# Optimization experiments

Measured on AMD Instinct MI355X. Metric: run time of the kernel, lower is better.

## Reference

```python
import jax, jax.numpy as jnp
import numpy as np

B, NU, NT = 128, 32, 64          # batch, users/sample, antennas/sample
IN_F, H, OUT_F, NL = 128, 128, 16, 2
N_U, N_A = B * NU, B * NT        # total user / antenna nodes


def setup_inputs() -> dict:
    key = jax.random.key(0)
    ks = iter(jax.random.split(key, 40))
    p = lambda shape: jax.random.normal(next(ks), shape, jnp.float32) * 0.05
    inp = {
        'user_feat': jax.random.normal(next(ks), (N_U, IN_F), jnp.float32),
        'ant_noise': jax.random.normal(next(ks), (N_A, H), jnp.float32),
    }
    # complete bipartite edges within each batch sample
    b = np.arange(B)[:, None, None]
    u = np.arange(NU)[None, :, None]
    t = np.arange(NT)[None, None, :]
    su = np.broadcast_to(b * NU + u, (B, NU, NT)).reshape(-1)  # user global ids
    dt = np.broadcast_to(b * NT + t, (B, NU, NT)).reshape(-1)  # antenna global ids
    inp['src_u2a'] = jnp.asarray(su, jnp.int32)
    inp['dst_u2a'] = jnp.asarray(dt, jnp.int32)
    inp['src_a2u'] = jnp.asarray(dt, jnp.int32)
    inp['dst_a2u'] = jnp.asarray(su, jnp.int32)
    inp['W_ue'] = p((IN_F, H)); inp['b_ue'] = p((H,))
    inp['W_t'] = p((H, H));     inp['b_t'] = p((H,))
    for name in ['ca_aggr', 'ca_self', 'ca_comb', 'cu_aggr', 'cu_self', 'cu_comb']:
        inp[name + '_W'] = p((NL, H, H))
        inp[name + '_b'] = p((NL, H))
    inp['W_norm'] = p((H, OUT_F)); inp['b_norm'] = p((OUT_F,))
    return inp


def mlp(x, W, b):
    # stack of NL Linear(H,H) + ReLU, as in MLP module
    for i in range(W.shape[0]):
        x = jax.nn.relu(x @ W[i] + b[i])
    return x


def rel_conv(src_f, dst_f, src_idx, dst_idx, n_dst, aW, ab, sW, sb, cW, cb):
    # GraphConv2: mean-aggregate mlp_aggr(src) over in-edges, combine with mlp_self(dst)
    msg = mlp(src_f, aW, ab)                                   # [n_src, H]
    summed = jax.ops.segment_sum(msg[src_idx], dst_idx, num_segments=n_dst)
    deg = jax.ops.segment_sum(jnp.ones(dst_idx.shape, jnp.float32), dst_idx,
                              num_segments=n_dst)
    mean = summed / jnp.maximum(deg, 1.0)[:, None]
    return mlp(mlp(dst_f, sW, sb) + mean, cW, cb)


def reference(user_feat, ant_noise, src_u2a, dst_u2a, src_a2u, dst_a2u,
              W_ue, b_ue, W_t, b_t,
              ca_aggr_W, ca_aggr_b, ca_self_W, ca_self_b, ca_comb_W, ca_comb_b,
              cu_aggr_W, cu_aggr_b, cu_self_W, cu_self_b, cu_comb_W, cu_comb_b,
              W_norm, b_norm):
    # InitLayer
    hu = jax.nn.relu(user_feat @ W_ue + b_ue)                  # [B*NU, H]
    ant = jax.nn.relu(hu.reshape(B, NU, H).mean(axis=1) @ W_t + b_t)  # [B, H]
    ha = jnp.repeat(ant, NT, axis=0) + ant_noise               # [B*NT, H]
    # two applications of the SAME HeteroGraphConv (shared weights)
    for _ in range(2):
        na = rel_conv(hu, ha, src_u2a, dst_u2a, N_A,
                      ca_aggr_W, ca_aggr_b, ca_self_W, ca_self_b, ca_comb_W, ca_comb_b)
        nu = rel_conv(ha, hu, src_a2u, dst_a2u, N_U,
                      cu_aggr_W, cu_aggr_b, cu_self_W, cu_self_b, cu_comb_W, cu_comb_b)
        hu, ha = nu, na
    # NormLayer: project, split real/imag, normalize to unit modulus
    y = (ha @ W_norm + b_norm).reshape(B, NT, OUT_F)
    rf = OUT_F // 2
    re, im = y[..., :rf], y[..., rf:]
    mag = jnp.sqrt(re * re + im * im)
    return jnp.concatenate([re / mag, im / mag], axis=-1)      # [B, NT, OUT_F]
```

## Files before the change

kernel.cpp:

```cpp
#include <hip/hip_runtime.h>
#include <math.h>


using frag  = __attribute__((ext_vector_type(8))) short;
using f32x4 = __attribute__((ext_vector_type(4))) float;

#define LDST 136
#define SCOPE_AGT __HIP_MEMORY_SCOPE_AGENT

__device__ __forceinline__ float  bf2f(ushort u) { return __uint_as_float(((unsigned)u) << 16); }
__device__ __forceinline__ ushort f2bf(float f) {
    unsigned u = __float_as_uint(f);
    u += 0x7fff + ((u >> 16) & 1);
    return (ushort)(u >> 16);
}
__device__ __forceinline__ unsigned cvtpk(float lo, float hi) {
    unsigned r;
    asm("v_cvt_pk_bf16_f32 %0, %1, %2" : "=v"(r) : "v"(lo), "v"(hi));
    return r;
}
__device__ __forceinline__ void gst16_sc(void* p, f32x4 v) {
    asm volatile("global_store_dwordx4 %0, %1, off sc1" :: "v"(p), "v"(v) : "memory");
}

struct GP {
    const float *uf, *noise, *b_ue, *W_t, *b_t;
    const float *bias6[6];
    const float *Wn, *bn;
    const ushort *Wp;
    float *out;
    float *pE, *pA0, *pU0, *pA1;
    unsigned *flg;
};

struct PrepP { const float* Wm[13]; ushort* Wp; unsigned* flg; };

__global__ __launch_bounds__(512) void k_prep(PrepP Q)
{
    const int tid = threadIdx.x, blk = blockIdx.x;
    if (blk < 16) Q.flg[blk * 512 + tid] = 0;
    const int e = (blk * 512 + tid) * 8;
    const int l = (e >> 3) & 63, w = (e >> 9) & 7, kc = (e >> 12) & 3, m = e >> 14;
    const float* src = Q.Wm[m] + (kc * 32 + (l >> 4) * 8) * 128 + w * 16 + (l & 15);
    ushort h[8];
#pragma unroll
    for (int j = 0; j < 8; ++j) h[j] = f2bf(src[j * 128]);
    uint4 o = { (unsigned)h[0] | ((unsigned)h[1] << 16), (unsigned)h[2] | ((unsigned)h[3] << 16),
                (unsigned)h[4] | ((unsigned)h[5] << 16), (unsigned)h[6] | ((unsigned)h[7] << 16) };
    *(uint4*)(Q.Wp + e) = o;
}

__device__ __forceinline__ void psync(unsigned* myf, unsigned* pf, unsigned s) {
    asm volatile("s_waitcnt vmcnt(0)" ::: "memory");
    __syncthreads();
    if (threadIdx.x == 0) {
        __hip_atomic_store(myf, s, __ATOMIC_RELAXED, SCOPE_AGT);
        while (__hip_atomic_load(pf, __ATOMIC_RELAXED, SCOPE_AGT) < s)
            __builtin_amdgcn_s_sleep(1);
    }
    __syncthreads();
}

struct AF { frag f[4]; };
__device__ __forceinline__ AF ldA(const ushort* __restrict__ Wp, int mat, int tid)
{
    AF a;
    const ushort* base = Wp + ((size_t)mat << 14) + (tid << 3);
#pragma unroll
    for (int kc = 0; kc < 4; ++kc)
        a.f[kc] = *(const frag*)(base + (kc << 12));
    return a;
}

template<int MT, bool MEANADD, bool CS>
__device__ __forceinline__ void mlp_stage(const AF& A, const ushort* Xl, ushort* Yl,
    const float* biasL, const float* meanL, float* csL, float* __restrict__ csG,
    int n0, int l15, int q)
{
    const float4 bv = *(const float4*)(biasL + n0 + q * 4);
    float4 mv = {0.f, 0.f, 0.f, 0.f};
    if (MEANADD) mv = *(const float4*)(meanL + n0 + q * 4);
    float cs0 = 0.f, cs1 = 0.f, cs2 = 0.f, cs3 = 0.f;
#pragma unroll
    for (int mt = 0; mt < MT; ++mt) {
        frag Bv[4];
#pragma unroll
        for (int kc = 0; kc < 4; ++kc)
            Bv[kc] = *(const frag*)(Xl + (mt * 16 + l15) * LDST + kc * 32 + q * 8);
        f32x4 acc = {0.f, 0.f, 0.f, 0.f};
#pragma unroll
        for (int kc = 0; kc < 4; ++kc)
            acc = __builtin_amdgcn_mfma_f32_16x16x32_bf16(A.f[kc], Bv[kc], acc, 0, 0, 0);
        float v0 = acc[0] + bv.x, v1 = acc[1] + bv.y, v2 = acc[2] + bv.z, v3 = acc[3] + bv.w;
        v0 = v0 > 0.f ? v0 : 0.f; v1 = v1 > 0.f ? v1 : 0.f;
        v2 = v2 > 0.f ? v2 : 0.f; v3 = v3 > 0.f ? v3 : 0.f;
        if (MEANADD) { v0 += mv.x; v1 += mv.y; v2 += mv.z; v3 += mv.w; }
        if (CS) { cs0 += v0; cs1 += v1; cs2 += v2; cs3 += v3; }
        uint2 o = { cvtpk(v0, v1), cvtpk(v2, v3) };
        *(uint2*)(Yl + (mt * 16 + l15) * LDST + n0 + q * 4) = o;
    }
    if (CS) {
#pragma unroll
        for (int m = 1; m <= 8; m <<= 1) {
            cs0 += __shfl_xor(cs0, m); cs1 += __shfl_xor(cs1, m);
            cs2 += __shfl_xor(cs2, m); cs3 += __shfl_xor(cs3, m);
        }
        if (l15 == 0) {
            f32x4 t = { cs0, cs1, cs2, cs3 };
            *(f32x4*)(csL + n0 + q * 4) = t;
            gst16_sc(csG + n0 + q * 4, t);
        }
    }
}

__global__ __launch_bounds__(512, 1) void k_gnn(GP P)
{
    __shared__ __align__(16) ushort HU[16 * LDST];
    __shared__ __align__(16) ushort HA[32 * LDST];
    __shared__ __align__(16) ushort T0[32 * LDST];
    __shared__ __align__(16) ushort T1[32 * LDST];
    __shared__ __align__(16) float  biasL[1792];
    __shared__ __align__(16) float  redL[512];
    __shared__ __align__(16) float  meanP[128], meanQ[128], antL[128];

    const int blk = blockIdx.x, tid = threadIdx.x;
    const int b = blk & 127, half = blk >> 7, prt = blk ^ 128;
    const int lane = tid & 63, wave = tid >> 6;
    const int q = lane >> 4, l15 = lane & 15;
    const int n0 = wave * 16;
    unsigned* myf = P.flg + blk * 32;
    unsigned* prf = P.flg + prt * 32;

    AF An = ldA(P.Wp, 12, tid);

    {
        const int r = tid >> 5, k4 = tid & 31;
        const float4 v = *(const float4*)(P.uf + (size_t)(b * 32 + half * 16 + r) * 128 + k4 * 4);
        uint2 o = { cvtpk(v.x, v.y), cvtpk(v.z, v.w) };
        *(uint2*)(T0 + r * LDST + k4 * 4) = o;
    }
#pragma unroll
    for (int c = tid; c < 1024; c += 512) {
        const int r = c >> 5, k4 = c & 31;
        const float4 v = *(const float4*)(P.noise + (size_t)(b * 64 + half * 32 + r) * 128 + k4 * 4);
        uint2 o = { cvtpk(v.x, v.y), cvtpk(v.z, v.w) };
        *(uint2*)(HA + r * LDST + k4 * 4) = o;
    }
    if (tid < 128) biasL[tid] = P.b_ue[tid];
    if (tid < 128) biasL[1664 + tid] = P.b_t[tid];
#pragma unroll
    for (int r = 0; r < 6; ++r)
        if (tid < 256) biasL[128 + r * 256 + tid] = P.bias6[r][tid];
    __syncthreads();

    AF A;
    A = An; An = ldA(P.Wp, 0, tid);
    mlp_stage<1, false, true>(A, T0, HU, biasL + 0, nullptr, meanP, P.pE + blk * 128, n0, l15, q);
    __syncthreads();
    A = An; An = ldA(P.Wp, 1, tid);
    mlp_stage<1, false, false>(A, HU, T0, biasL + 128, nullptr, nullptr, nullptr, n0, l15, q);
    __syncthreads();
    A = An; An = ldA(P.Wp, 6, tid);
    mlp_stage<1, false, true>(A, T0, T1, biasL + 256, nullptr, meanQ, P.pA0 + blk * 128, n0, l15, q);
    __syncthreads();
    psync(myf, prf, 1u);

    if (tid < 128) {
        meanP[tid] = (meanP[tid] + P.pE[prt * 128 + tid]) * (1.f / 32.f);
        meanQ[tid] = (meanQ[tid] + P.pA0[prt * 128 + tid]) * (1.f / 32.f);
    }
    __syncthreads();
    {
        const int g = tid >> 7, col = tid & 127;
        float s = 0.f;
#pragma unroll 4
        for (int k = g * 32; k < g * 32 + 32; ++k) s += meanP[k] * P.W_t[k * 128 + col];
        redL[g * 128 + col] = s;
    }
    __syncthreads();
    if (tid < 128) {
        float a = biasL[1664 + tid] + redL[tid] + redL[128 + tid] + redL[256 + tid] + redL[384 + tid];
        antL[tid] = a > 0.f ? a : 0.f;
    }
    __syncthreads();
#pragma unroll
    for (int c = tid; c < 1024; c += 512) {
        const int r = c >> 5, k4 = c & 31;
        ushort4 h = *(ushort4*)(HA + r * LDST + k4 * 4);
        uint2 o = { cvtpk(bf2f(h.x) + antL[k4 * 4 + 0], bf2f(h.y) + antL[k4 * 4 + 1]),
                    cvtpk(bf2f(h.z) + antL[k4 * 4 + 2], bf2f(h.w) + antL[k4 * 4 + 3]) };
        *(uint2*)(HA + r * LDST + k4 * 4) = o;
    }
    __syncthreads();

    A = An; An = ldA(P.Wp, 7, tid);
    mlp_stage<2, false, false>(A, HA, T0, biasL + 896, nullptr, nullptr, nullptr, n0, l15, q);
    __syncthreads();
    A = An; An = ldA(P.Wp, 2, tid);
    mlp_stage<2, false, true>(A, T0, T1, biasL + 1024, nullptr, meanP, P.pU0 + blk * 128, n0, l15, q);
    __syncthreads();
    A = An; An = ldA(P.Wp, 3, tid);
    mlp_stage<2, false, false>(A, HA, T0, biasL + 384, nullptr, nullptr, nullptr, n0, l15, q);
    __syncthreads();
    psync(myf, prf, 2u);
    if (tid < 128)
        meanP[tid] = (meanP[tid] + P.pU0[prt * 128 + tid]) * (1.f / 64.f);
    __syncthreads();
    A = An; An = ldA(P.Wp, 4, tid);
    mlp_stage<2, true , false>(A, T0, T1, biasL + 512, meanQ, nullptr, nullptr, n0, l15, q);
    __syncthreads();
    A = An; An = ldA(P.Wp, 5, tid);
    mlp_stage<2, false, false>(A, T1, T0, biasL + 640, nullptr, nullptr, nullptr, n0, l15, q);
    __syncthreads();
    A = An; An = ldA(P.Wp, 8, tid);
    mlp_stage<2, false, false>(A, T0, HA, biasL + 768, nullptr, nullptr, nullptr, n0, l15, q);
    __syncthreads();
    A = An; An = ldA(P.Wp, 9, tid);
    mlp_stage<1, false, false>(A, HU, T0, biasL + 1152, nullptr, nullptr, nullptr, n0, l15, q);
    __syncthreads();
    A = An; An = ldA(P.Wp, 10, tid);
    mlp_stage<1, true , false>(A, T0, T1, biasL + 1280, meanP, nullptr, nullptr, n0, l15, q);
    __syncthreads();
    A = An; An = ldA(P.Wp, 11, tid);
    mlp_stage<1, false, false>(A, T1, T0, biasL + 1408, nullptr, nullptr, nullptr, n0, l15, q);
    __syncthreads();
    A = An; An = ldA(P.Wp, 0, tid);
    mlp_stage<1, false, false>(A, T0, HU, biasL + 1536, nullptr, nullptr, nullptr, n0, l15, q);
    __syncthreads();

    A = An; An = ldA(P.Wp, 1, tid);
    mlp_stage<1, false, false>(A, HU, T0, biasL + 128, nullptr, nullptr, nullptr, n0, l15, q);
    __syncthreads();
    A = An; An = ldA(P.Wp, 2, tid);
    mlp_stage<1, false, true>(A, T0, T1, biasL + 256, nullptr, meanQ, P.pA1 + blk * 128, n0, l15, q);
    __syncthreads();
    A = An; An = ldA(P.Wp, 3, tid);
    mlp_stage<2, false, false>(A, HA, T0, biasL + 384, nullptr, nullptr, nullptr, n0, l15, q);
    __syncthreads();
    psync(myf, prf, 3u);
    if (tid < 128)
        meanQ[tid] = (meanQ[tid] + P.pA1[prt * 128 + tid]) * (1.f / 32.f);
    __syncthreads();
    A = An; An = ldA(P.Wp, 4, tid);
    mlp_stage<2, true , false>(A, T0, T1, biasL + 512, meanQ, nullptr, nullptr, n0, l15, q);
    __syncthreads();
    A = An; An = ldA(P.Wp, 5, tid);
    mlp_stage<2, false, false>(A, T1, T0, biasL + 640, nullptr, nullptr, nullptr, n0, l15, q);
    __syncthreads();
    A = An;
    mlp_stage<2, false, false>(A, T0, T1, biasL + 768, nullptr, nullptr, nullptr, n0, l15, q);
    __syncthreads();

    float* WnS = (float*)T0;
    *(float4*)(WnS + tid * 4) = *(const float4*)(P.Wn + tid * 4);
    __syncthreads();
    {
        const int row = tid >> 4, j = tid & 15;
        float acc = P.bn[j];
        const uint4* h4 = (const uint4*)(T1 + row * LDST);
#pragma unroll
        for (int kb = 0; kb < 16; ++kb) {
            const uint4 u = h4[kb];
            const float* wp = WnS + kb * 128 + j;
            acc += bf2f((ushort)u.x) * wp[0]   + bf2f((ushort)(u.x >> 16)) * wp[16]
                 + bf2f((ushort)u.y) * wp[32]  + bf2f((ushort)(u.y >> 16)) * wp[48]
                 + bf2f((ushort)u.z) * wp[64]  + bf2f((ushort)(u.z >> 16)) * wp[80]
                 + bf2f((ushort)u.w) * wp[96]  + bf2f((ushort)(u.w >> 16)) * wp[112];
        }
        const float other = __shfl_xor(acc, 8);
        const float mag = sqrtf(acc * acc + other * other);
        P.out[(size_t)(b * 64 + half * 32 + row) * 16 + j] = acc / mag;
    }
}

extern "C" void kernel_launch(void* const* d_in, const int* in_sizes, int n_in,
                              void* d_out, int out_size, void* d_ws, size_t ws_size,
                              hipStream_t stream)
{
    GP P;
    P.uf    = (const float*)d_in[0];
    P.noise = (const float*)d_in[1];
    const float* W_ue = (const float*)d_in[6];
    P.b_ue  = (const float*)d_in[7];
    P.W_t   = (const float*)d_in[8];
    P.b_t   = (const float*)d_in[9];
    const float* caW[3] = {(const float*)d_in[10], (const float*)d_in[12], (const float*)d_in[14]};
    const float* cab[3] = {(const float*)d_in[11], (const float*)d_in[13], (const float*)d_in[15]};
    const float* cuW[3] = {(const float*)d_in[16], (const float*)d_in[18], (const float*)d_in[20]};
    const float* cub[3] = {(const float*)d_in[17], (const float*)d_in[19], (const float*)d_in[21]};
    P.Wn  = (const float*)d_in[22];
    P.bn  = (const float*)d_in[23];
    P.out = (float*)d_out;

    PrepP Q;
    Q.Wm[0]  = caW[0]; Q.Wm[1]  = caW[0] + 16384;
    Q.Wm[2]  = caW[1]; Q.Wm[3]  = caW[1] + 16384;
    Q.Wm[4]  = caW[2]; Q.Wm[5]  = caW[2] + 16384;
    Q.Wm[6]  = cuW[0]; Q.Wm[7]  = cuW[0] + 16384;
    Q.Wm[8]  = cuW[1]; Q.Wm[9]  = cuW[1] + 16384;
    Q.Wm[10] = cuW[2]; Q.Wm[11] = cuW[2] + 16384;
    Q.Wm[12] = W_ue;
    P.bias6[0] = cab[0]; P.bias6[1] = cab[1]; P.bias6[2] = cab[2];
    P.bias6[3] = cub[0]; P.bias6[4] = cub[1]; P.bias6[5] = cub[2];

    char* w = (char*)d_ws;
    P.flg = (unsigned*)w;
    P.pE  = (float*)(w + 32768);
    P.pA0 = P.pE  + 256 * 128;
    P.pU0 = P.pA0 + 256 * 128;
    P.pA1 = P.pU0 + 256 * 128;
    ushort* Wp = (ushort*)(w + 32768 + 4 * 256 * 128 * 4);
    Q.Wp = Wp;
    Q.flg = P.flg;
    P.Wp = Wp;

    k_prep<<<dim3(52), dim3(512), 0, stream>>>(Q);
    k_gnn<<<dim3(256), dim3(512), 0, stream>>>(P);
}
```

Before: 120.6 us.

## Split each batch sample across four workgroups instead of two

Each sample's work is now split across four cooperating workgroups instead of two, giving 512 blocks. Each block handles 8 users and 16 antennas, and column-sum partials are exchanged through a four-way flag sync. The goal is to fill more of the GPU's compute units and shorten the serial MLP chain per block. In exchange, user-side MFMA tiles are half empty (8 valid rows out of 16), more blocks take part in each sync, and per-sample global partial traffic grows.

New measurement: 126.8 us. +5.2%, slower.

```diff
diff --git a/kernel.cpp b/kernel.cpp
--- a/kernel.cpp
+++ b/kernel.cpp
@@ -38,7 +38,7 @@
 __global__ __launch_bounds__(512) void k_prep(PrepP Q)
 {
     const int tid = threadIdx.x, blk = blockIdx.x;
-    if (blk < 16) Q.flg[blk * 512 + tid] = 0;
+    if (blk < 32) Q.flg[blk * 512 + tid] = 0;
     const int e = (blk * 512 + tid) * 8;
     const int l = (e >> 3) & 63, w = (e >> 9) & 7, kc = (e >> 12) & 3, m = e >> 14;
     const float* src = Q.Wm[m] + (kc * 32 + (l >> 4) * 8) * 128 + w * 16 + (l & 15);
@@ -50,11 +50,13 @@
     *(uint4*)(Q.Wp + e) = o;
 }
 
-__device__ __forceinline__ void psync(unsigned* myf, unsigned* pf, unsigned s) {
+__device__ __forceinline__ void psync4(unsigned* flg, int blk, unsigned s) {
     asm volatile("s_waitcnt vmcnt(0)" ::: "memory");
     __syncthreads();
-    if (threadIdx.x == 0) {
-        __hip_atomic_store(myf, s, __ATOMIC_RELAXED, SCOPE_AGT);
+    if (threadIdx.x < 3) {
+        if (threadIdx.x == 0)
+            __hip_atomic_store(flg + blk * 32, s, __ATOMIC_RELAXED, SCOPE_AGT);
+        unsigned* pf = flg + (((blk + 128 * (threadIdx.x + 1)) & 511) * 32);
         while (__hip_atomic_load(pf, __ATOMIC_RELAXED, SCOPE_AGT) < s)
             __builtin_amdgcn_s_sleep(1);
     }
@@ -72,7 +74,7 @@
     return a;
 }
 
-template<int MT, bool MEANADD, bool CS>
+template<int VALID, bool MEANADD, bool CS>
 __device__ __forceinline__ void mlp_stage(const AF& A, const ushort* Xl, ushort* Yl,
     const float* biasL, const float* meanL, float* csL, float* __restrict__ csG,
     int n0, int l15, int q)
@@ -80,26 +82,26 @@
     const float4 bv = *(const float4*)(biasL + n0 + q * 4);
     float4 mv = {0.f, 0.f, 0.f, 0.f};
     if (MEANADD) mv = *(const float4*)(meanL + n0 + q * 4);
-    float cs0 = 0.f, cs1 = 0.f, cs2 = 0.f, cs3 = 0.f;
-#pragma unroll
-    for (int mt = 0; mt < MT; ++mt) {
-        frag Bv[4];
-#pragma unroll
-        for (int kc = 0; kc < 4; ++kc)
-            Bv[kc] = *(const frag*)(Xl + (mt * 16 + l15) * LDST + kc * 32 + q * 8);
-        f32x4 acc = {0.f, 0.f, 0.f, 0.f};
-#pragma unroll
-        for (int kc = 0; kc < 4; ++kc)
-            acc = __builtin_amdgcn_mfma_f32_16x16x32_bf16(A.f[kc], Bv[kc], acc, 0, 0, 0);
-        float v0 = acc[0] + bv.x, v1 = acc[1] + bv.y, v2 = acc[2] + bv.z, v3 = acc[3] + bv.w;
-        v0 = v0 > 0.f ? v0 : 0.f; v1 = v1 > 0.f ? v1 : 0.f;
-        v2 = v2 > 0.f ? v2 : 0.f; v3 = v3 > 0.f ? v3 : 0.f;
-        if (MEANADD) { v0 += mv.x; v1 += mv.y; v2 += mv.z; v3 += mv.w; }
-        if (CS) { cs0 += v0; cs1 += v1; cs2 += v2; cs3 += v3; }
+    frag Bv[4];
+#pragma unroll
+    for (int kc = 0; kc < 4; ++kc)
+        Bv[kc] = *(const frag*)(Xl + l15 * LDST + kc * 32 + q * 8);
+    f32x4 acc = {0.f, 0.f, 0.f, 0.f};
+#pragma unroll
+    for (int kc = 0; kc < 4; ++kc)
+        acc = __builtin_amdgcn_mfma_f32_16x16x32_bf16(A.f[kc], Bv[kc], acc, 0, 0, 0);
+    float v0 = acc[0] + bv.x, v1 = acc[1] + bv.y, v2 = acc[2] + bv.z, v3 = acc[3] + bv.w;
+    v0 = v0 > 0.f ? v0 : 0.f; v1 = v1 > 0.f ? v1 : 0.f;
+    v2 = v2 > 0.f ? v2 : 0.f; v3 = v3 > 0.f ? v3 : 0.f;
+    if (MEANADD) { v0 += mv.x; v1 += mv.y; v2 += mv.z; v3 += mv.w; }
+    const bool vr = (VALID == 16) || (l15 < VALID);
+    if (vr) {
         uint2 o = { cvtpk(v0, v1), cvtpk(v2, v3) };
-        *(uint2*)(Yl + (mt * 16 + l15) * LDST + n0 + q * 4) = o;
+        *(uint2*)(Yl + l15 * LDST + n0 + q * 4) = o;
     }
     if (CS) {
+        float cs0 = vr ? v0 : 0.f, cs1 = vr ? v1 : 0.f,
+              cs2 = vr ? v2 : 0.f, cs3 = vr ? v3 : 0.f;
 #pragma unroll
         for (int m = 1; m <= 8; m <<= 1) {
             cs0 += __shfl_xor(cs0, m); cs1 += __shfl_xor(cs1, m);
@@ -113,36 +115,35 @@
     }
 }
 
-__global__ __launch_bounds__(512, 1) void k_gnn(GP P)
+__global__ __launch_bounds__(512, 4) void k_gnn(GP P)
 {
     __shared__ __align__(16) ushort HU[16 * LDST];
-    __shared__ __align__(16) ushort HA[32 * LDST];
-    __shared__ __align__(16) ushort T0[32 * LDST];
-    __shared__ __align__(16) ushort T1[32 * LDST];
+    __shared__ __align__(16) ushort HA[16 * LDST];
+    __shared__ __align__(16) ushort T0[16 * LDST];
+    __shared__ __align__(16) ushort T1[16 * LDST];
     __shared__ __align__(16) float  biasL[1792];
     __shared__ __align__(16) float  redL[512];
+    __shared__ __align__(16) float  WnS[2048];
     __shared__ __align__(16) float  meanP[128], meanQ[128], antL[128];
 
     const int blk = blockIdx.x, tid = threadIdx.x;
-    const int b = blk & 127, half = blk >> 7, prt = blk ^ 128;
+    const int b = blk & 127, qt = blk >> 7;
+    const int p1 = (blk + 128) & 511, p2 = (blk + 256) & 511, p3 = (blk + 384) & 511;
     const int lane = tid & 63, wave = tid >> 6;
     const int q = lane >> 4, l15 = lane & 15;
     const int n0 = wave * 16;
-    unsigned* myf = P.flg + blk * 32;
-    unsigned* prf = P.flg + prt * 32;
 
     AF An = ldA(P.Wp, 12, tid);
 
+    if (tid < 256) {
+        const int r = tid >> 5, k4 = tid & 31;
+        const float4 v = *(const float4*)(P.uf + (size_t)(b * 32 + qt * 8 + r) * 128 + k4 * 4);
+        uint2 o = { cvtpk(v.x, v.y), cvtpk(v.z, v.w) };
+        *(uint2*)(T0 + r * LDST + k4 * 4) = o;
+    }
     {
         const int r = tid >> 5, k4 = tid & 31;
-        const float4 v = *(const float4*)(P.uf + (size_t)(b * 32 + half * 16 + r) * 128 + k4 * 4);
-        uint2 o = { cvtpk(v.x, v.y), cvtpk(v.z, v.w) };
-        *(uint2*)(T0 + r * LDST + k4 * 4) = o;
-    }
-#pragma unroll
-    for (int c = tid; c < 1024; c += 512) {
-        const int r = c >> 5, k4 = c & 31;
-        const float4 v = *(const float4*)(P.noise + (size_t)(b * 64 + half * 32 + r) * 128 + k4 * 4);
+        const float4 v = *(const float4*)(P.noise + (size_t)(b * 64 + qt * 16 + r) * 128 + k4 * 4);
         uint2 o = { cvtpk(v.x, v.y), cvtpk(v.z, v.w) };
         *(uint2*)(HA + r * LDST + k4 * 4) = o;
     }
@@ -155,19 +156,21 @@
 
     AF A;
     A = An; An = ldA(P.Wp, 0, tid);
-    mlp_stage<1, false, true>(A, T0, HU, biasL + 0, nullptr, meanP, P.pE + blk * 128, n0, l15, q);
+    mlp_stage<8, false, true>(A, T0, HU, biasL + 0, nullptr, meanP, P.pE + blk * 128, n0, l15, q);
     __syncthreads();
     A = An; An = ldA(P.Wp, 1, tid);
-    mlp_stage<1, false, false>(A, HU, T0, biasL + 128, nullptr, nullptr, nullptr, n0, l15, q);
+    mlp_stage<8, false, false>(A, HU, T0, biasL + 128, nullptr, nullptr, nullptr, n0, l15, q);
     __syncthreads();
     A = An; An = ldA(P.Wp, 6, tid);
-    mlp_stage<1, false, true>(A, T0, T1, biasL + 256, nullptr, meanQ, P.pA0 + blk * 128, n0, l15, q);
-    __syncthreads();
-    psync(myf, prf, 1u);
+    mlp_stage<8, false, true>(A, T0, T1, biasL + 256, nullptr, meanQ, P.pA0 + blk * 128, n0, l15, q);
+    __syncthreads();
+    psync4(P.flg, blk, 1u);
 
     if (tid < 128) {
-        meanP[tid] = (meanP[tid] + P.pE[prt * 128 + tid]) * (1.f / 32.f);
-        meanQ[tid] = (meanQ[tid] + P.pA0[prt * 128 + tid]) * (1.f / 32.f);
+        meanP[tid] = (meanP[tid] + P.pE[p1 * 128 + tid] + P.pE[p2 * 128 + tid]
+                                 + P.pE[p3 * 128 + tid]) * (1.f / 32.f);
+        meanQ[tid] = (meanQ[tid] + P.pA0[p1 * 128 + tid] + P.pA0[p2 * 128 + tid]
+                                 + P.pA0[p3 * 128 + tid]) * (1.f / 32.f);
     }
     __syncthreads();
     {
@@ -183,9 +186,8 @@
         antL[tid] = a > 0.f ? a : 0.f;
     }
     __syncthreads();
-#pragma unroll
-    for (int c = tid; c < 1024; c += 512) {
-        const int r = c >> 5, k4 = c & 31;
+    {
+        const int r = tid >> 5, k4 = tid & 31;
         ushort4 h = *(ushort4*)(HA + r * LDST + k4 * 4);
         uint2 o = { cvtpk(bf2f(h.x) + antL[k4 * 4 + 0], bf2f(h.y) + antL[k4 * 4 + 1]),
                     cvtpk(bf2f(h.z) + antL[k4 * 4 + 2], bf2f(h.w) + antL[k4 * 4 + 3]) };
@@ -194,67 +196,68 @@
     __syncthreads();
 
     A = An; An = ldA(P.Wp, 7, tid);
-    mlp_stage<2, false, false>(A, HA, T0, biasL + 896, nullptr, nullptr, nullptr, n0, l15, q);
+    mlp_stage<16, false, false>(A, HA, T0, biasL + 896, nullptr, nullptr, nullptr, n0, l15, q);
     __syncthreads();
     A = An; An = ldA(P.Wp, 2, tid);
-    mlp_stage<2, false, true>(A, T0, T1, biasL + 1024, nullptr, meanP, P.pU0 + blk * 128, n0, l15, q);
+    mlp_stage<16, false, true>(A, T0, T1, biasL + 1024, nullptr, meanP, P.pU0 + blk * 128, n0, l15, q);
     __syncthreads();
     A = An; An = ldA(P.Wp, 3, tid);
-    mlp_stage<2, false, false>(A, HA, T0, biasL + 384, nullptr, nullptr, nullptr, n0, l15, q);
-    __syncthreads();
-    psync(myf, prf, 2u);
+    mlp_stage<16, false, false>(A, HA, T0, biasL + 384, nullptr, nullptr, nullptr, n0, l15, q);
+    __syncthreads();
+    psync4(P.flg, blk, 2u);
     if (tid < 128)
-        meanP[tid] = (meanP[tid] + P.pU0[prt * 128 + tid]) * (1.f / 64.f);
+        meanP[tid] = (meanP[tid] + P.pU0[p1 * 128 + tid] + P.pU0[p2 * 128 + tid]
+                                 + P.pU0[p3 * 128 + tid]) * (1.f / 64.f);
     __syncthreads();
     A = An; An = ldA(P.Wp, 4, tid);
-    mlp_stage<2, true , false>(A, T0, T1, biasL + 512, meanQ, nullptr, nullptr, n0, l15, q);
+    mlp_stage<16, true , false>(A, T0, T1, biasL + 512, meanQ, nullptr, nullptr, n0, l15, q);
     __syncthreads();
     A = An; An = ldA(P.Wp, 5, tid);
-    mlp_stage<2, false, false>(A, T1, T0, biasL + 640, nullptr, nullptr, nullptr, n0, l15, q);
+    mlp_stage<16, false, false>(A, T1, T0, biasL + 640, nullptr, nullptr, nullptr, n0, l15, q);
     __syncthreads();
     A = An; An = ldA(P.Wp, 8, tid);
-    mlp_stage<2, false, false>(A, T0, HA, biasL + 768, nullptr, nullptr, nullptr, n0, l15, q);
+    mlp_stage<16, false, false>(A, T0, HA, biasL + 768, nullptr, nullptr, nullptr, n0, l15, q);
     __syncthreads();
     A = An; An = ldA(P.Wp, 9, tid);
-    mlp_stage<1, false, false>(A, HU, T0, biasL + 1152, nullptr, nullptr, nullptr, n0, l15, q);
+    mlp_stage<8, false, false>(A, HU, T0, biasL + 1152, nullptr, nullptr, nullptr, n0, l15, q);
     __syncthreads();
     A = An; An = ldA(P.Wp, 10, tid);
-    mlp_stage<1, true , false>(A, T0, T1, biasL + 1280, meanP, nullptr, nullptr, n0, l15, q);
+    mlp_stage<8, true , false>(A, T0, T1, biasL + 1280, meanP, nullptr, nullptr, n0, l15, q);
     __syncthreads();
     A = An; An = ldA(P.Wp, 11, tid);
-    mlp_stage<1, false, false>(A, T1, T0, biasL + 1408, nullptr, nullptr, nullptr, n0, l15, q);
+    mlp_stage<8, false, false>(A, T1, T0, biasL + 1408, nullptr, nullptr, nullptr, n0, l15, q);
     __syncthreads();
     A = An; An = ldA(P.Wp, 0, tid);
-    mlp_stage<1, false, false>(A, T0, HU, biasL + 1536, nullptr, nullptr, nullptr, n0, l15, q);
+    mlp_stage<8, false, false>(A, T0, HU, biasL + 1536, nullptr, nullptr, nullptr, n0, l15, q);
     __syncthreads();
 
     A = An; An = ldA(P.Wp, 1, tid);
-    mlp_stage<1, false, false>(A, HU, T0, biasL + 128, nullptr, nullptr, nullptr, n0, l15, q);
+    mlp_stage<8, false, false>(A, HU, T0, biasL + 128, nullptr, nullptr, nullptr, n0, l15, q);
     __syncthreads();
     A = An; An = ldA(P.Wp, 2, tid);
-    mlp_stage<1, false, true>(A, T0, T1, biasL + 256, nullptr, meanQ, P.pA1 + blk * 128, n0, l15, q);
+    mlp_stage<8, false, true>(A, T0, T1, biasL + 256, nullptr, meanQ, P.pA1 + blk * 128, n0, l15, q);
     __syncthreads();
     A = An; An = ldA(P.Wp, 3, tid);
-    mlp_stage<2, false, false>(A, HA, T0, biasL + 384, nullptr, nullptr, nullptr, n0, l15, q);
-    __syncthreads();
-    psync(myf, prf, 3u);
+    mlp_stage<16, false, false>(A, HA, T0, biasL + 384, nullptr, nullptr, nullptr, n0, l15, q);
+    __syncthreads();
+    psync4(P.flg, blk, 3u);
     if (tid < 128)
-        meanQ[tid] = (meanQ[tid] + P.pA1[prt * 128 + tid]) * (1.f / 32.f);
+        meanQ[tid] = (meanQ[tid] + P.pA1[p1 * 128 + tid] + P.pA1[p2 * 128 + tid]
+                                 + P.pA1[p3 * 128 + tid]) * (1.f / 32.f);
     __syncthreads();
     A = An; An = ldA(P.Wp, 4, tid);
-    mlp_stage<2, true , false>(A, T0, T1, biasL + 512, meanQ, nullptr, nullptr, n0, l15, q);
+    mlp_stage<16, true , false>(A, T0, T1, biasL + 512, meanQ, nullptr, nullptr, n0, l15, q);
     __syncthreads();
     A = An; An = ldA(P.Wp, 5, tid);
-    mlp_stage<2, false, false>(A, T1, T0, biasL + 640, nullptr, nullptr, nullptr, n0, l15, q);
+    mlp_stage<16, false, false>(A, T1, T0, biasL + 640, nullptr, nullptr, nullptr, n0, l15, q);
     __syncthreads();
     A = An;
-    mlp_stage<2, false, false>(A, T0, T1, biasL + 768, nullptr, nullptr, nullptr, n0, l15, q);
-    __syncthreads();
-
-    float* WnS = (float*)T0;
+    mlp_stage<16, false, false>(A, T0, T1, biasL + 768, nullptr, nullptr, nullptr, n0, l15, q);
+    __syncthreads();
+
     *(float4*)(WnS + tid * 4) = *(const float4*)(P.Wn + tid * 4);
     __syncthreads();
-    {
+    if (tid < 256) {
         const int row = tid >> 4, j = tid & 15;
         float acc = P.bn[j];
         const uint4* h4 = (const uint4*)(T1 + row * LDST);
@@ -269,7 +272,7 @@
         }
         const float other = __shfl_xor(acc, 8);
         const float mag = sqrtf(acc * acc + other * other);
-        P.out[(size_t)(b * 64 + half * 32 + row) * 16 + j] = acc / mag;
+        P.out[(size_t)(b * 64 + qt * 16 + row) * 16 + j] = acc / mag;
     }
 }
 
@@ -305,15 +308,15 @@
 
     char* w = (char*)d_ws;
     P.flg = (unsigned*)w;
-    P.pE  = (float*)(w + 32768);
-    P.pA0 = P.pE  + 256 * 128;
-    P.pU0 = P.pA0 + 256 * 128;
-    P.pA1 = P.pU0 + 256 * 128;
-    ushort* Wp = (ushort*)(w + 32768 + 4 * 256 * 128 * 4);
+    P.pE  = (float*)(w + 65536);
+    P.pA0 = P.pE  + 512 * 128;
+    P.pU0 = P.pA0 + 512 * 128;
+    P.pA1 = P.pU0 + 512 * 128;
+    ushort* Wp = (ushort*)(w + 65536 + 4 * 512 * 128 * 4);
     Q.Wp = Wp;
     Q.flg = P.flg;
     P.Wp = Wp;
 
     k_prep<<<dim3(52), dim3(512), 0, stream>>>(Q);
-    k_gnn<<<dim3(256), dim3(512), 0, stream>>>(P);
-}
+    k_gnn<<<dim3(512), dim3(512), 0, stream>>>(P);
+}
```
